# Kernel tuning notes

Hardware: AMD Instinct MI355X
Metric: run time of the kernel (lower is better)

The kernel has to match this reference:

```python
import jax, jax.numpy as jnp
import numpy as np

N_NODES = 100000
N_GRAPHS = 64
NEG_SLOPE = 0.1


def lrelu(x):
    return jnp.where(x > 0, x, NEG_SLOPE * x)


def gcn_layer(x, W, b, src, dst, deg_inv_sqrt):
    # PyG GCNConv: x' = D^-1/2 (A + I) D^-1/2 (x W) + b
    h = x @ W  # [N, out]
    norm = (deg_inv_sqrt[src] * deg_inv_sqrt[dst])[:, None]  # [E, 1]
    agg = jax.ops.segment_sum(h[src] * norm, dst, num_segments=N_NODES)
    agg = agg + h * (deg_inv_sqrt ** 2)[:, None]  # self-loop contribution
    return agg + b


def setup_inputs() -> dict:
    key = jax.random.key(0)
    ks = jax.random.split(key, 12)
    E = 1600000
    x = jax.random.normal(ks[0], (N_NODES, 128), dtype=jnp.float32)
    edge_index = jax.random.randint(ks[1], (2, E), 0, N_NODES, dtype=jnp.int32)
    batch = jnp.sort(jax.random.randint(ks[2], (N_NODES,), 0, N_GRAPHS, dtype=jnp.int32))

    def glorot(k, shape):
        fan_in, fan_out = shape
        s = jnp.sqrt(6.0 / (fan_in + fan_out))
        return jax.random.uniform(k, shape, jnp.float32, -s, s)

    return {
        "x": x,
        "edge_index": edge_index,
        "batch": batch,
        "W1": glorot(ks[3], (128, 32)),
        "b1": jnp.zeros((32,), jnp.float32),
        "W2": glorot(ks[4], (32, 64)),
        "b2": jnp.zeros((64,), jnp.float32),
        "Wl1": glorot(ks[5], (64, 128)),
        "bl1": jnp.zeros((128,), jnp.float32),
        "Wl2": glorot(ks[6], (128, 64)),
        "bl2": jnp.zeros((64,), jnp.float32),
        "Wl3": glorot(ks[7], (64, 1)),
        "bl3": jnp.zeros((1,), jnp.float32),
    }


def reference(x, edge_index, batch, W1, b1, W2, b2, Wl1, bl1, Wl2, bl2, Wl3, bl3):
    src, dst = edge_index[0], edge_index[1]
    # degree with self-loops (symmetric norm, all edge weights = 1)
    deg = jax.ops.segment_sum(jnp.ones_like(src, dtype=x.dtype), dst, num_segments=N_NODES) + 1.0
    deg_inv_sqrt = jax.lax.rsqrt(deg)

    h = lrelu(gcn_layer(x, W1, b1, src, dst, deg_inv_sqrt))
    h = gcn_layer(h, W2, b2, src, dst, deg_inv_sqrt)
    g = jax.ops.segment_max(h, batch, num_segments=N_GRAPHS)  # global max pool [G, 64]
    g = lrelu(g @ Wl1 + bl1)
    g = lrelu(g @ Wl2 + bl2)
    return g @ Wl3 + bl3  # [G, 1]
```

## Files before the change

kernel.cpp:

```cpp
#include <hip/hip_runtime.h>
#include <hip/hip_fp16.h>
#include <math.h>

#define N_NODES 100000
#define N_EDGES 1600000
#define N_GRAPHS 64
#define NB 391
#define CAP 5504

__device__ __forceinline__ unsigned f2o(float f) {
    unsigned u = __float_as_uint(f);
    return (u & 0x80000000u) ? ~u : (u | 0x80000000u);
}
__device__ __forceinline__ float o2f(unsigned u) {
    return (u & 0x80000000u) ? __uint_as_float(u & 0x7fffffffu) : __uint_as_float(~u);
}

__device__ __forceinline__ float4 cvt8(float2 raw) {
    __half2 h0 = ((const __half2*)&raw)[0];
    __half2 h1 = ((const __half2*)&raw)[1];
    float2 f0 = __half22float2(h0);
    float2 f1 = __half22float2(h1);
    return make_float4(f0.x, f0.y, f1.x, f1.y);
}
__device__ __forceinline__ float4 loadh8(const __half* p) {
    return cvt8(*(const float2*)p);
}
__device__ __forceinline__ void storeh8(__half* p, float4 v) {
    __half2 o0 = __floats2half2_rn(v.x, v.y);
    __half2 o1 = __floats2half2_rn(v.z, v.w);
    float2 ow;
    ((__half2*)&ow)[0] = o0;
    ((__half2*)&ow)[1] = o1;
    *(float2*)p = ow;
}

typedef _Float16 h2r __attribute__((ext_vector_type(2)));
typedef _Float16 h4  __attribute__((ext_vector_type(4)));
union HB { float4 f4; h2r h[4]; };
union H4 { float2 f2; h4 h; };

__global__ __launch_bounds__(256) void bucket_kernel(const int* __restrict__ src, const int* __restrict__ dst,
                                                     int* __restrict__ bucketCursor, unsigned* __restrict__ ebuf) {
    __shared__ int hist[NB];
    __shared__ int cur[NB];
    int tid = threadIdx.x;
    for (int b = tid; b < NB; b += 256) hist[b] = 0;
    __syncthreads();
    int e0 = blockIdx.x * 3200;
    for (int i = tid; i < 3200; i += 256) {
        int d = dst[e0 + i];
        atomicAdd(&hist[d >> 8], 1);
    }
    __syncthreads();
    for (int b = tid; b < NB; b += 256) {
        int h = hist[b];
        cur[b] = h ? atomicAdd(&bucketCursor[b], h) : 0;
    }
    __syncthreads();
    for (int i = tid; i < 3200; i += 256) {
        int d = dst[e0 + i];
        int s = src[e0 + i];
        int bu = d >> 8;
        int pos = atomicAdd(&cur[bu], 1);
        if (pos < CAP)
            ebuf[(size_t)bu * CAP + pos] = ((unsigned)(d & 255) << 24) | (unsigned)s;
    }
}

__global__ __launch_bounds__(256) void csr_kernel(const unsigned* __restrict__ ebuf,
                                                  const int* __restrict__ bucketCursor,
                                                  int* __restrict__ colb, int* __restrict__ rowptr,
                                                  int* __restrict__ cnt, float* __restrict__ dis) {
    __shared__ unsigned stage[CAP];
    __shared__ int c256[256], row256[256], cur256[256];
    int b = blockIdx.x;
    int tid = threadIdx.x;
    int M = bucketCursor[b];
    if (M > CAP) M = CAP;
    c256[tid] = 0;
    __syncthreads();
    const unsigned* eb = ebuf + (size_t)b * CAP;
    for (int i = tid; i < M; i += 256) atomicAdd(&c256[eb[i] >> 24], 1);
    __syncthreads();
    if (tid < 64) {
        int c0 = c256[tid * 4], c1 = c256[tid * 4 + 1], c2 = c256[tid * 4 + 2], c3 = c256[tid * 4 + 3];
        int s = c0 + c1 + c2 + c3;
        int inc = s;
        #pragma unroll
        for (int o = 1; o < 64; o <<= 1) {
            int v = __shfl_up(inc, o, 64);
            if (tid >= o) inc += v;
        }
        int ex = inc - s;
        row256[tid * 4] = ex;
        row256[tid * 4 + 1] = ex + c0;
        row256[tid * 4 + 2] = ex + c0 + c1;
        row256[tid * 4 + 3] = ex + c0 + c1 + c2;
    }
    __syncthreads();
    cur256[tid] = row256[tid];
    int node = (b << 8) + tid;
    if (node < N_NODES) {
        int c = c256[tid];
        cnt[node] = c;
        dis[node] = rsqrtf((float)(c + 1));
        rowptr[node] = b * CAP + row256[tid];
    }
    __syncthreads();
    for (int i = tid; i < M; i += 256) {
        unsigned p = eb[i];
        int slot = atomicAdd(&cur256[p >> 24], 1);
        stage[slot] = p & 0xFFFFFFu;
    }
    __syncthreads();
    for (int i = tid; i < M; i += 256) colb[b * CAP + i] = (int)stage[i];
}

__global__ __launch_bounds__(256) void gemm1_kernel(const float* __restrict__ x, const float* __restrict__ W1,
                                                    const float* __restrict__ dis, __half* __restrict__ hs1h) {
    __shared__ __half xsh[128][136];
    __shared__ __half wth[32][136];
    int tid = threadIdx.x;
    int r0 = blockIdx.x * 128;
    for (int idx = tid; idx < 128 * 32; idx += 256) {
        int k = idx >> 5, j = idx & 31;
        wth[j][k] = __float2half_rn(W1[idx]);
    }
    for (int idx = tid; idx < 128 * 32; idx += 256) {
        int r = idx >> 5, c4 = idx & 31;
        int gr = r0 + r;
        float4 v = (gr < N_NODES) ? ((const float4*)x)[(size_t)gr * 32 + c4] : make_float4(0.f, 0.f, 0.f, 0.f);
        __half* p = &xsh[r][c4 * 4];
        *(__half2*)p       = __floats2half2_rn(v.x, v.y);
        *(__half2*)(p + 2) = __floats2half2_rn(v.z, v.w);
    }
    __syncthreads();
    int jg = tid & 7;
    int rg = tid >> 3;
    float acc[4][4];
    #pragma unroll
    for (int i = 0; i < 4; i++)
        #pragma unroll
        for (int j = 0; j < 4; j++) acc[i][j] = 0.f;
    for (int kc = 0; kc < 128; kc += 8) {
        HB xr[4], wr[4];
        #pragma unroll
        for (int ri = 0; ri < 4; ri++) xr[ri].f4 = *(const float4*)&xsh[rg + 32 * ri][kc];
        #pragma unroll
        for (int jj = 0; jj < 4; jj++) wr[jj].f4 = *(const float4*)&wth[jg * 4 + jj][kc];
        #pragma unroll
        for (int ri = 0; ri < 4; ri++) {
            #pragma unroll
            for (int jj = 0; jj < 4; jj++) {
                #pragma unroll
                for (int t = 0; t < 4; t++) {
#if defined(__has_builtin) && __has_builtin(__builtin_amdgcn_fdot2)
                    acc[ri][jj] = __builtin_amdgcn_fdot2(xr[ri].h[t], wr[jj].h[t], acc[ri][jj], false);
#else
                    acc[ri][jj] += (float)xr[ri].h[t][0] * (float)wr[jj].h[t][0]
                                 + (float)xr[ri].h[t][1] * (float)wr[jj].h[t][1];
#endif
                }
            }
        }
    }
    #pragma unroll
    for (int ri = 0; ri < 4; ri++) {
        int gr = r0 + rg + 32 * ri;
        if (gr < N_NODES) {
            float dr = dis[gr];
            float2 ow;
            ((__half2*)&ow)[0] = __floats2half2_rn(dr * acc[ri][0], dr * acc[ri][1]);
            ((__half2*)&ow)[1] = __floats2half2_rn(dr * acc[ri][2], dr * acc[ri][3]);
            *(float2*)&hs1h[(size_t)gr * 32 + jg * 4] = ow;
        }
    }
}

__global__ __launch_bounds__(256) void agg1_kernel(const __half* __restrict__ hs1h, const int* __restrict__ colb,
                                                   const int* __restrict__ rowptr, const int* __restrict__ cnt,
                                                   const float* __restrict__ dis, const float* __restrict__ b1,
                                                   __half* __restrict__ t1h) {
    int tid = threadIdx.x;
    int wid = tid >> 6;
    int lane = tid & 63;
    int half = lane >> 5;
    int es = (lane >> 3) & 3;
    int q = lane & 7;
    int w = blockIdx.x * 4 + wid;
    int r0 = w * 4;

    H4 z; z.f2 = make_float2(0.f, 0.f);
    int r = r0 + half;
    int st = rowptr[r];
    int n = cnt[r];
    H4 pS = z, p0 = z, p1 = z, p2 = z, p3 = z, p4 = z, p5 = z;
    if (es == 0) pS.f2 = *(const float2*)(hs1h + (size_t)r * 32 + q * 4);
    {
        int e0 = es, e1 = 4 + es, e2 = 8 + es, e3 = 12 + es, e4 = 16 + es, e5 = 20 + es;
        if (e0 < n) p0.f2 = *(const float2*)(hs1h + (size_t)colb[st + e0] * 32 + q * 4);
        if (e1 < n) p1.f2 = *(const float2*)(hs1h + (size_t)colb[st + e1] * 32 + q * 4);
        if (e2 < n) p2.f2 = *(const float2*)(hs1h + (size_t)colb[st + e2] * 32 + q * 4);
        if (e3 < n) p3.f2 = *(const float2*)(hs1h + (size_t)colb[st + e3] * 32 + q * 4);
        if (e4 < n) p4.f2 = *(const float2*)(hs1h + (size_t)colb[st + e4] * 32 + q * 4);
        if (e5 < n) p5.f2 = *(const float2*)(hs1h + (size_t)colb[st + e5] * 32 + q * 4);
    }
    #pragma unroll
    for (int i = 0; i < 2; i++) {
        int rA = r;
        int stA = st, nA = n;
        H4 rS = pS, v0 = p0, v1 = p1, v2 = p2, v3 = p3, v4 = p4, v5 = p5;
        pS = z; p0 = z; p1 = z; p2 = z; p3 = z; p4 = z; p5 = z;
        if (i == 0) {
            r = r0 + 2 + half;
            st = rowptr[r];
            n = cnt[r];
            if (es == 0) pS.f2 = *(const float2*)(hs1h + (size_t)r * 32 + q * 4);
            int e0 = es, e1 = 4 + es, e2 = 8 + es, e3 = 12 + es, e4 = 16 + es, e5 = 20 + es;
            if (e0 < n) p0.f2 = *(const float2*)(hs1h + (size_t)colb[st + e0] * 32 + q * 4);
            if (e1 < n) p1.f2 = *(const float2*)(hs1h + (size_t)colb[st + e1] * 32 + q * 4);
            if (e2 < n) p2.f2 = *(const float2*)(hs1h + (size_t)colb[st + e2] * 32 + q * 4);
            if (e3 < n) p3.f2 = *(const float2*)(hs1h + (size_t)colb[st + e3] * 32 + q * 4);
            if (e4 < n) p4.f2 = *(const float2*)(hs1h + (size_t)colb[st + e4] * 32 + q * 4);
            if (e5 < n) p5.f2 = *(const float2*)(hs1h + (size_t)colb[st + e5] * 32 + q * 4);
        }
        h4 sh = (rS.h + (v0.h + v1.h)) + ((v2.h + v3.h) + (v4.h + v5.h));
        float4 a = make_float4((float)sh.x, (float)sh.y, (float)sh.z, (float)sh.w);
        for (int k = 24; k < nA; k += 8) {
            int e0 = k + es, e1 = k + 4 + es;
            if (e0 < nA) {
                float4 v = loadh8(hs1h + (size_t)colb[stA + e0] * 32 + q * 4);
                a.x += v.x; a.y += v.y; a.z += v.z; a.w += v.w;
            }
            if (e1 < nA) {
                float4 v = loadh8(hs1h + (size_t)colb[stA + e1] * 32 + q * 4);
                a.x += v.x; a.y += v.y; a.z += v.z; a.w += v.w;
            }
        }
        #pragma unroll
        for (int m = 8; m <= 16; m <<= 1) {
            a.x += __shfl_xor(a.x, m, 64);
            a.y += __shfl_xor(a.y, m, 64);
            a.z += __shfl_xor(a.z, m, 64);
            a.w += __shfl_xor(a.w, m, 64);
        }
        if (es == 0) {
            float4 bv = *(const float4*)&b1[q * 4];
            float dr = dis[rA];
            float4 v;
            v.x = dr * a.x + bv.x; v.y = dr * a.y + bv.y; v.z = dr * a.z + bv.z; v.w = dr * a.w + bv.w;
            v.x = v.x > 0.f ? v.x : 0.1f * v.x;
            v.y = v.y > 0.f ? v.y : 0.1f * v.y;
            v.z = v.z > 0.f ? v.z : 0.1f * v.z;
            v.w = v.w > 0.f ? v.w : 0.1f * v.w;
            v.x *= dr; v.y *= dr; v.z *= dr; v.w *= dr;
            storeh8(t1h + (size_t)rA * 32 + q * 4, v);
        }
    }
}

__global__ __launch_bounds__(1024) void agg2gemm_kernel(const __half* __restrict__ t1h, const int* __restrict__ colb,
                                                        const int* __restrict__ rowptr, const int* __restrict__ cnt,
                                                        const float* __restrict__ dis,
                                                        const float* __restrict__ W2, const float* __restrict__ b2,
                                                        const int* __restrict__ batch, unsigned* __restrict__ gbufu) {
    __shared__ float as1[64][32];
    __shared__ float w2s[32][64];
    __shared__ float red[16][64];
    int tid = threadIdx.x;
    int r0 = blockIdx.x * 64;
    for (int idx = tid; idx < 32 * 64; idx += 1024) w2s[idx >> 6][idx & 63] = W2[idx];

    int wid = tid >> 6;
    int lane = tid & 63;
    int half = lane >> 5;
    int es = (lane >> 3) & 3;
    int q = lane & 7;
    int base = r0 + wid * 4;

    H4 z; z.f2 = make_float2(0.f, 0.f);
    int r = base + half;
    bool vld = r < N_NODES;
    int st = vld ? rowptr[r] : 0;
    int n  = vld ? cnt[r] : 0;
    H4 pS = z, p0 = z, p1 = z, p2 = z, p3 = z, p4 = z, p5 = z;
    if (vld && es == 0) pS.f2 = *(const float2*)(t1h + (size_t)r * 32 + q * 4);
    {
        int e0 = es, e1 = 4 + es, e2 = 8 + es, e3 = 12 + es, e4 = 16 + es, e5 = 20 + es;
        if (e0 < n) p0.f2 = *(const float2*)(t1h + (size_t)colb[st + e0] * 32 + q * 4);
        if (e1 < n) p1.f2 = *(const float2*)(t1h + (size_t)colb[st + e1] * 32 + q * 4);
        if (e2 < n) p2.f2 = *(const float2*)(t1h + (size_t)colb[st + e2] * 32 + q * 4);
        if (e3 < n) p3.f2 = *(const float2*)(t1h + (size_t)colb[st + e3] * 32 + q * 4);
        if (e4 < n) p4.f2 = *(const float2*)(t1h + (size_t)colb[st + e4] * 32 + q * 4);
        if (e5 < n) p5.f2 = *(const float2*)(t1h + (size_t)colb[st + e5] * 32 + q * 4);
    }
    #pragma unroll
    for (int i = 0; i < 2; i++) {
        int rA = i * 2;
        int rAg = base + rA + half;
        bool vA = rAg < N_NODES;
        int stA = st, nA = n;
        H4 rS = pS, v0 = p0, v1 = p1, v2 = p2, v3 = p3, v4 = p4, v5 = p5;
        pS = z; p0 = z; p1 = z; p2 = z; p3 = z; p4 = z; p5 = z;
        if (i == 0) {
            r = base + 2 + half;
            vld = r < N_NODES;
            st = vld ? rowptr[r] : 0;
            n  = vld ? cnt[r] : 0;
            if (vld && es == 0) pS.f2 = *(const float2*)(t1h + (size_t)r * 32 + q * 4);
            int e0 = es, e1 = 4 + es, e2 = 8 + es, e3 = 12 + es, e4 = 16 + es, e5 = 20 + es;
            if (e0 < n) p0.f2 = *(const float2*)(t1h + (size_t)colb[st + e0] * 32 + q * 4);
            if (e1 < n) p1.f2 = *(const float2*)(t1h + (size_t)colb[st + e1] * 32 + q * 4);
            if (e2 < n) p2.f2 = *(const float2*)(t1h + (size_t)colb[st + e2] * 32 + q * 4);
            if (e3 < n) p3.f2 = *(const float2*)(t1h + (size_t)colb[st + e3] * 32 + q * 4);
            if (e4 < n) p4.f2 = *(const float2*)(t1h + (size_t)colb[st + e4] * 32 + q * 4);
            if (e5 < n) p5.f2 = *(const float2*)(t1h + (size_t)colb[st + e5] * 32 + q * 4);
        }
        h4 sh = (rS.h + (v0.h + v1.h)) + ((v2.h + v3.h) + (v4.h + v5.h));
        float4 a = make_float4((float)sh.x, (float)sh.y, (float)sh.z, (float)sh.w);
        for (int k = 24; k < nA; k += 8) {
            int e0 = k + es, e1 = k + 4 + es;
            if (e0 < nA) {
                float4 v = loadh8(t1h + (size_t)colb[stA + e0] * 32 + q * 4);
                a.x += v.x; a.y += v.y; a.z += v.z; a.w += v.w;
            }
            if (e1 < nA) {
                float4 v = loadh8(t1h + (size_t)colb[stA + e1] * 32 + q * 4);
                a.x += v.x; a.y += v.y; a.z += v.z; a.w += v.w;
            }
        }
        #pragma unroll
        for (int m = 8; m <= 16; m <<= 1) {
            a.x += __shfl_xor(a.x, m, 64);
            a.y += __shfl_xor(a.y, m, 64);
            a.z += __shfl_xor(a.z, m, 64);
            a.w += __shfl_xor(a.w, m, 64);
        }
        if (es == 0 && vA) {
            float dr = dis[rAg];
            float4 o = make_float4(dr * a.x, dr * a.y, dr * a.z, dr * a.w);
            *(float4*)&as1[wid * 4 + rA + half][q * 4] = o;
        }
    }
    __syncthreads();

    int j = tid & 63;
    int rq = tid >> 6;
    float w2c[32];
    #pragma unroll
    for (int k = 0; k < 32; k++) w2c[k] = w2s[k][j];
    float bj = b2[j];
    int rend = (r0 + 64 <= N_NODES) ? 64 : (N_NODES - r0);
    int gfirst = batch[r0];
    int glast = batch[r0 + rend - 1];
    bool uni = (gfirst == glast);
    float runmax = -INFINITY;
    #pragma unroll
    for (int i = 0; i < 4; i++) {
        int rl = rq + i * 16;
        if (rl >= rend) break;
        float acc = bj;
        #pragma unroll
        for (int kc = 0; kc < 32; kc += 4) {
            float4 av = *(const float4*)&as1[rl][kc];
            acc += av.x * w2c[kc] + av.y * w2c[kc + 1] + av.z * w2c[kc + 2] + av.w * w2c[kc + 3];
        }
        if (uni) runmax = fmaxf(runmax, acc);
        else atomicMax(&gbufu[batch[r0 + rl] * 64 + j], f2o(acc));
    }
    if (uni) {
        red[rq][j] = runmax;
        __syncthreads();
        if (tid < 64) {
            float m = -INFINITY;
            #pragma unroll
            for (int k = 0; k < 16; k++) m = fmaxf(m, red[k][tid]);
            atomicMax(&gbufu[gfirst * 64 + tid], f2o(m));
        }
    }
}

__global__ __launch_bounds__(256) void mlp_kernel(const unsigned* __restrict__ gbufu,
                                                  const float* __restrict__ Wl1, const float* __restrict__ bl1,
                                                  const float* __restrict__ Wl2, const float* __restrict__ bl2,
                                                  const float* __restrict__ Wl3, const float* __restrict__ bl3,
                                                  float* __restrict__ out) {
    __shared__ float A[64][64];
    __shared__ float B[64][128];
    int tid = threadIdx.x;
    for (int idx = tid; idx < 64 * 64; idx += 256) A[idx >> 6][idx & 63] = o2f(gbufu[idx]);
    __syncthreads();
    {
        int j = tid & 127;
        int rg = tid >> 7;
        float wc[64];
        #pragma unroll
        for (int k = 0; k < 64; k++) wc[k] = Wl1[k * 128 + j];
        float bj = bl1[j];
        for (int r = rg; r < 64; r += 2) {
            float acc = bj;
            #pragma unroll
            for (int kc = 0; kc < 64; kc += 4) {
                float4 av = *(const float4*)&A[r][kc];
                acc += av.x * wc[kc] + av.y * wc[kc + 1] + av.z * wc[kc + 2] + av.w * wc[kc + 3];
            }
            B[r][j] = acc > 0.f ? acc : 0.1f * acc;
        }
    }
    __syncthreads();
    {
        int j = tid & 63;
        int rg = tid >> 6;
        float wc[128];
        #pragma unroll
        for (int k = 0; k < 128; k++) wc[k] = Wl2[k * 64 + j];
        float bj = bl2[j];
        for (int r = rg; r < 64; r += 4) {
            float acc = bj;
            #pragma unroll
            for (int kc = 0; kc < 128; kc += 4) {
                float4 bv = *(const float4*)&B[r][kc];
                acc += bv.x * wc[kc] + bv.y * wc[kc + 1] + bv.z * wc[kc + 2] + bv.w * wc[kc + 3];
            }
            A[r][j] = acc > 0.f ? acc : 0.1f * acc;
        }
    }
    __syncthreads();
    if (tid < 64) {
        int r = tid;
        float acc = bl3[0];
        #pragma unroll
        for (int k = 0; k < 64; k++) acc += A[r][k] * Wl3[k];
        out[r] = acc;
    }
}

extern "C" void kernel_launch(void* const* d_in, const int* in_sizes, int n_in,
                              void* d_out, int out_size, void* d_ws, size_t ws_size,
                              hipStream_t stream) {
    (void)in_sizes; (void)n_in; (void)out_size; (void)ws_size;
    const float* x    = (const float*)d_in[0];
    const int*   edge = (const int*)d_in[1];
    const int*   batch= (const int*)d_in[2];
    const float* W1   = (const float*)d_in[3];
    const float* b1   = (const float*)d_in[4];
    const float* W2   = (const float*)d_in[5];
    const float* b2   = (const float*)d_in[6];
    const float* Wl1  = (const float*)d_in[7];
    const float* bl1  = (const float*)d_in[8];
    const float* Wl2  = (const float*)d_in[9];
    const float* bl2  = (const float*)d_in[10];
    const float* Wl3  = (const float*)d_in[11];
    const float* bl3  = (const float*)d_in[12];
    const int* srcp = edge;
    const int* dstp = edge + N_EDGES;

    char* ws = (char*)d_ws;
    int*      bucketCursor = (int*)ws;
    unsigned* gbufu        = (unsigned*)(bucketCursor + NB);
    size_t zeroed = (size_t)(NB + N_GRAPHS * 64) * 4;
    size_t off = (zeroed + 255) & ~(size_t)255;
    auto alloc = [&](size_t bytes) { char* p = ws + off; off = (off + bytes + 255) & ~(size_t)255; return p; };
    float*    dis    = (float*)alloc((size_t)N_NODES * 4);
    int*      cnt    = (int*)alloc((size_t)N_NODES * 4);
    int*      rowptr = (int*)alloc((size_t)N_NODES * 4);
    unsigned* ebuf   = (unsigned*)alloc((size_t)NB * CAP * 4);
    int*      colb   = (int*)alloc((size_t)NB * CAP * 4);
    __half*   hs1h   = (__half*)alloc((size_t)N_NODES * 32 * 2);
    __half*   t1h    = (__half*)alloc((size_t)N_NODES * 32 * 2);

    hipMemsetAsync(ws, 0, zeroed, stream);

    bucket_kernel  <<<500, 256, 0, stream>>>(srcp, dstp, bucketCursor, ebuf);
    csr_kernel     <<<NB, 256, 0, stream>>>(ebuf, bucketCursor, colb, rowptr, cnt, dis);
    gemm1_kernel   <<<(N_NODES + 127) / 128, 256, 0, stream>>>(x, W1, dis, hs1h);
    agg1_kernel    <<<6250, 256, 0, stream>>>(hs1h, colb, rowptr, cnt, dis, b1, t1h);
    agg2gemm_kernel<<<(N_NODES + 63) / 64, 1024, 0, stream>>>(t1h, colb, rowptr, cnt, dis, W2, b2, batch, gbufu);
    mlp_kernel     <<<1, 256, 0, stream>>>(gbufu, Wl1, bl1, Wl2, bl2, Wl3, bl3, (float*)d_out);
}
```

Measured before the change: 261.5 us.

## Split 32-wide half feature arrays into two 16-wide halves for gathers

Stores the layer-1 hidden features and the layer-1 output as two separate 16-column half-precision arrays instead of one 32-column array. The aggregation kernels now gather each half in a separate pass, using 4 lanes per row and 8 edges in parallel. The intent is a smaller per-pass gather working set (1.6 MB per half) that fits better in cache and raises edge-level parallelism. In exchange, colb indices are read twice and each gather is a narrower 32-byte access, so the number of random row fetches doubles.

```diff
diff --git a/kernel.cpp b/kernel.cpp
--- a/kernel.cpp
+++ b/kernel.cpp
@@ -118,7 +118,8 @@
 }
 
 __global__ __launch_bounds__(256) void gemm1_kernel(const float* __restrict__ x, const float* __restrict__ W1,
-                                                    const float* __restrict__ dis, __half* __restrict__ hs1h) {
+                                                    const float* __restrict__ dis,
+                                                    __half* __restrict__ ha, __half* __restrict__ hb) {
     __shared__ __half xsh[128][136];
     __shared__ __half wth[32][136];
     int tid = threadIdx.x;
@@ -165,6 +166,8 @@
             }
         }
     }
+    __half* hp = (jg < 4) ? ha : hb;
+    int q4 = (jg & 3) * 4;
     #pragma unroll
     for (int ri = 0; ri < 4; ri++) {
         int gr = r0 + rg + 32 * ri;
@@ -173,81 +176,77 @@
             float2 ow;
             ((__half2*)&ow)[0] = __floats2half2_rn(dr * acc[ri][0], dr * acc[ri][1]);
             ((__half2*)&ow)[1] = __floats2half2_rn(dr * acc[ri][2], dr * acc[ri][3]);
-            *(float2*)&hs1h[(size_t)gr * 32 + jg * 4] = ow;
-        }
-    }
-}
-
-__global__ __launch_bounds__(256) void agg1_kernel(const __half* __restrict__ hs1h, const int* __restrict__ colb,
+            *(float2*)&hp[(size_t)gr * 16 + q4] = ow;
+        }
+    }
+}
+
+__global__ __launch_bounds__(256) void agg1_kernel(const __half* __restrict__ ha, const __half* __restrict__ hb,
+                                                   const int* __restrict__ colb,
                                                    const int* __restrict__ rowptr, const int* __restrict__ cnt,
                                                    const float* __restrict__ dis, const float* __restrict__ b1,
-                                                   __half* __restrict__ t1h) {
+                                                   __half* __restrict__ ta, __half* __restrict__ tb) {
     int tid = threadIdx.x;
     int wid = tid >> 6;
     int lane = tid & 63;
     int half = lane >> 5;
-    int es = (lane >> 3) & 3;
-    int q = lane & 7;
+    int es = (lane >> 2) & 7;
+    int q = lane & 3;
     int w = blockIdx.x * 4 + wid;
     int r0 = w * 4;
 
+    int rI[2]  = { r0 + half, r0 + 2 + half };
+    int stI[2] = { rowptr[rI[0]], rowptr[rI[1]] };
+    int nI[2]  = { cnt[rI[0]], cnt[rI[1]] };
+    float dI[2] = { dis[rI[0]], dis[rI[1]] };
+
     H4 z; z.f2 = make_float2(0.f, 0.f);
-    int r = r0 + half;
-    int st = rowptr[r];
-    int n = cnt[r];
-    H4 pS = z, p0 = z, p1 = z, p2 = z, p3 = z, p4 = z, p5 = z;
-    if (es == 0) pS.f2 = *(const float2*)(hs1h + (size_t)r * 32 + q * 4);
+    H4 pS = z, p0 = z, p1 = z, p2 = z;
     {
-        int e0 = es, e1 = 4 + es, e2 = 8 + es, e3 = 12 + es, e4 = 16 + es, e5 = 20 + es;
-        if (e0 < n) p0.f2 = *(const float2*)(hs1h + (size_t)colb[st + e0] * 32 + q * 4);
-        if (e1 < n) p1.f2 = *(const float2*)(hs1h + (size_t)colb[st + e1] * 32 + q * 4);
-        if (e2 < n) p2.f2 = *(const float2*)(hs1h + (size_t)colb[st + e2] * 32 + q * 4);
-        if (e3 < n) p3.f2 = *(const float2*)(hs1h + (size_t)colb[st + e3] * 32 + q * 4);
-        if (e4 < n) p4.f2 = *(const float2*)(hs1h + (size_t)colb[st + e4] * 32 + q * 4);
-        if (e5 < n) p5.f2 = *(const float2*)(hs1h + (size_t)colb[st + e5] * 32 + q * 4);
-    }
-    #pragma unroll
-    for (int i = 0; i < 2; i++) {
-        int rA = r;
-        int stA = st, nA = n;
-        H4 rS = pS, v0 = p0, v1 = p1, v2 = p2, v3 = p3, v4 = p4, v5 = p5;
-        pS = z; p0 = z; p1 = z; p2 = z; p3 = z; p4 = z; p5 = z;
-        if (i == 0) {
-            r = r0 + 2 + half;
-            st = rowptr[r];
-            n = cnt[r];
-            if (es == 0) pS.f2 = *(const float2*)(hs1h + (size_t)r * 32 + q * 4);
-            int e0 = es, e1 = 4 + es, e2 = 8 + es, e3 = 12 + es, e4 = 16 + es, e5 = 20 + es;
-            if (e0 < n) p0.f2 = *(const float2*)(hs1h + (size_t)colb[st + e0] * 32 + q * 4);
-            if (e1 < n) p1.f2 = *(const float2*)(hs1h + (size_t)colb[st + e1] * 32 + q * 4);
-            if (e2 < n) p2.f2 = *(const float2*)(hs1h + (size_t)colb[st + e2] * 32 + q * 4);
-            if (e3 < n) p3.f2 = *(const float2*)(hs1h + (size_t)colb[st + e3] * 32 + q * 4);
-            if (e4 < n) p4.f2 = *(const float2*)(hs1h + (size_t)colb[st + e4] * 32 + q * 4);
-            if (e5 < n) p5.f2 = *(const float2*)(hs1h + (size_t)colb[st + e5] * 32 + q * 4);
-        }
-        h4 sh = (rS.h + (v0.h + v1.h)) + ((v2.h + v3.h) + (v4.h + v5.h));
+        int st = stI[0], n = nI[0];
+        if (es == 0) pS.f2 = *(const float2*)(ha + (size_t)rI[0] * 16 + q * 4);
+        int e0 = es, e1 = 8 + es, e2 = 16 + es;
+        if (e0 < n) p0.f2 = *(const float2*)(ha + (size_t)colb[st + e0] * 16 + q * 4);
+        if (e1 < n) p1.f2 = *(const float2*)(ha + (size_t)colb[st + e1] * 16 + q * 4);
+        if (e2 < n) p2.f2 = *(const float2*)(ha + (size_t)colb[st + e2] * 16 + q * 4);
+    }
+    #pragma unroll
+    for (int s = 0; s < 4; ++s) {
+        int it = s & 1;
+        const __half* gpA = (s >> 1) ? hb : ha;
+        int stA = stI[it], nA = nI[it], rA = rI[it];
+        float drA = dI[it];
+        H4 rS = pS, v0 = p0, v1 = p1, v2 = p2;
+        pS = z; p0 = z; p1 = z; p2 = z;
+        if (s < 3) {
+            int itn = (s + 1) & 1;
+            const __half* gp = ((s + 1) >> 1) ? hb : ha;
+            int st = stI[itn], n = nI[itn];
+            if (es == 0) pS.f2 = *(const float2*)(gp + (size_t)rI[itn] * 16 + q * 4);
+            int e0 = es, e1 = 8 + es, e2 = 16 + es;
+            if (e0 < n) p0.f2 = *(const float2*)(gp + (size_t)colb[st + e0] * 16 + q * 4);
+            if (e1 < n) p1.f2 = *(const float2*)(gp + (size_t)colb[st + e1] * 16 + q * 4);
+            if (e2 < n) p2.f2 = *(const float2*)(gp + (size_t)colb[st + e2] * 16 + q * 4);
+        }
+        h4 sh = (rS.h + (v0.h + v1.h)) + v2.h;
         float4 a = make_float4((float)sh.x, (float)sh.y, (float)sh.z, (float)sh.w);
         for (int k = 24; k < nA; k += 8) {
-            int e0 = k + es, e1 = k + 4 + es;
-            if (e0 < nA) {
-                float4 v = loadh8(hs1h + (size_t)colb[stA + e0] * 32 + q * 4);
+            int e = k + es;
+            if (e < nA) {
+                float4 v = loadh8(gpA + (size_t)colb[stA + e] * 16 + q * 4);
                 a.x += v.x; a.y += v.y; a.z += v.z; a.w += v.w;
             }
-            if (e1 < nA) {
-                float4 v = loadh8(hs1h + (size_t)colb[stA + e1] * 32 + q * 4);
-                a.x += v.x; a.y += v.y; a.z += v.z; a.w += v.w;
-            }
-        }
-        #pragma unroll
-        for (int m = 8; m <= 16; m <<= 1) {
+        }
+        #pragma unroll
+        for (int m = 4; m <= 16; m <<= 1) {
             a.x += __shfl_xor(a.x, m, 64);
             a.y += __shfl_xor(a.y, m, 64);
             a.z += __shfl_xor(a.z, m, 64);
             a.w += __shfl_xor(a.w, m, 64);
         }
         if (es == 0) {
-            float4 bv = *(const float4*)&b1[q * 4];
-            float dr = dis[rA];
+            float4 bv = *(const float4*)&b1[((s >> 1) << 4) + q * 4];
+            float dr = drA;
             float4 v;
             v.x = dr * a.x + bv.x; v.y = dr * a.y + bv.y; v.z = dr * a.z + bv.z; v.w = dr * a.w + bv.w;
             v.x = v.x > 0.f ? v.x : 0.1f * v.x;
@@ -255,12 +254,14 @@
             v.z = v.z > 0.f ? v.z : 0.1f * v.z;
             v.w = v.w > 0.f ? v.w : 0.1f * v.w;
             v.x *= dr; v.y *= dr; v.z *= dr; v.w *= dr;
-            storeh8(t1h + (size_t)rA * 32 + q * 4, v);
-        }
-    }
-}
-
-__global__ __launch_bounds__(1024) void agg2gemm_kernel(const __half* __restrict__ t1h, const int* __restrict__ colb,
+            __half* op = ((s >> 1) ? tb : ta) + (size_t)rA * 16 + q * 4;
+            storeh8(op, v);
+        }
+    }
+}
+
+__global__ __launch_bounds__(1024) void agg2gemm_kernel(const __half* __restrict__ ta, const __half* __restrict__ tb,
+                                                        const int* __restrict__ colb,
                                                         const int* __restrict__ rowptr, const int* __restrict__ cnt,
                                                         const float* __restrict__ dis,
                                                         const float* __restrict__ W2, const float* __restrict__ b2,
@@ -275,72 +276,65 @@
     int wid = tid >> 6;
     int lane = tid & 63;
     int half = lane >> 5;
-    int es = (lane >> 3) & 3;
-    int q = lane & 7;
+    int es = (lane >> 2) & 7;
+    int q = lane & 3;
     int base = r0 + wid * 4;
 
+    int rI[2]  = { base + half, base + 2 + half };
+    bool vI[2] = { rI[0] < N_NODES, rI[1] < N_NODES };
+    int stI[2] = { vI[0] ? rowptr[rI[0]] : 0, vI[1] ? rowptr[rI[1]] : 0 };
+    int nI[2]  = { vI[0] ? cnt[rI[0]] : 0,   vI[1] ? cnt[rI[1]] : 0 };
+    float dI[2] = { vI[0] ? dis[rI[0]] : 0.f, vI[1] ? dis[rI[1]] : 0.f };
+
     H4 z; z.f2 = make_float2(0.f, 0.f);
-    int r = base + half;
-    bool vld = r < N_NODES;
-    int st = vld ? rowptr[r] : 0;
-    int n  = vld ? cnt[r] : 0;
-    H4 pS = z, p0 = z, p1 = z, p2 = z, p3 = z, p4 = z, p5 = z;
-    if (vld && es == 0) pS.f2 = *(const float2*)(t1h + (size_t)r * 32 + q * 4);
+    H4 pS = z, p0 = z, p1 = z, p2 = z;
     {
-        int e0 = es, e1 = 4 + es, e2 = 8 + es, e3 = 12 + es, e4 = 16 + es, e5 = 20 + es;
-        if (e0 < n) p0.f2 = *(const float2*)(t1h + (size_t)colb[st + e0] * 32 + q * 4);
-        if (e1 < n) p1.f2 = *(const float2*)(t1h + (size_t)colb[st + e1] * 32 + q * 4);
-        if (e2 < n) p2.f2 = *(const float2*)(t1h + (size_t)colb[st + e2] * 32 + q * 4);
-        if (e3 < n) p3.f2 = *(const float2*)(t1h + (size_t)colb[st + e3] * 32 + q * 4);
-        if (e4 < n) p4.f2 = *(const float2*)(t1h + (size_t)colb[st + e4] * 32 + q * 4);
-        if (e5 < n) p5.f2 = *(const float2*)(t1h + (size_t)colb[st + e5] * 32 + q * 4);
-    }
-    #pragma unroll
-    for (int i = 0; i < 2; i++) {
-        int rA = i * 2;
-        int rAg = base + rA + half;
-        bool vA = rAg < N_NODES;
-        int stA = st, nA = n;
-        H4 rS = pS, v0 = p0, v1 = p1, v2 = p2, v3 = p3, v4 = p4, v5 = p5;
-        pS = z; p0 = z; p1 = z; p2 = z; p3 = z; p4 = z; p5 = z;
-        if (i == 0) {
-            r = base + 2 + half;
-            vld = r < N_NODES;
-            st = vld ? rowptr[r] : 0;
-            n  = vld ? cnt[r] : 0;
-            if (vld && es == 0) pS.f2 = *(const float2*)(t1h + (size_t)r * 32 + q * 4);
-            int e0 = es, e1 = 4 + es, e2 = 8 + es, e3 = 12 + es, e4 = 16 + es, e5 = 20 + es;
-            if (e0 < n) p0.f2 = *(const float2*)(t1h + (size_t)colb[st + e0] * 32 + q * 4);
-            if (e1 < n) p1.f2 = *(const float2*)(t1h + (size_t)colb[st + e1] * 32 + q * 4);
-            if (e2 < n) p2.f2 = *(const float2*)(t1h + (size_t)colb[st + e2] * 32 + q * 4);
-            if (e3 < n) p3.f2 = *(const float2*)(t1h + (size_t)colb[st + e3] * 32 + q * 4);
-            if (e4 < n) p4.f2 = *(const float2*)(t1h + (size_t)colb[st + e4] * 32 + q * 4);
-            if (e5 < n) p5.f2 = *(const float2*)(t1h + (size_t)colb[st + e5] * 32 + q * 4);
-        }
-        h4 sh = (rS.h + (v0.h + v1.h)) + ((v2.h + v3.h) + (v4.h + v5.h));
+        int st = stI[0], n = nI[0];
+        if (vI[0] && es == 0) pS.f2 = *(const float2*)(ta + (size_t)rI[0] * 16 + q * 4);
+        int e0 = es, e1 = 8 + es, e2 = 16 + es;
+        if (e0 < n) p0.f2 = *(const float2*)(ta + (size_t)colb[st + e0] * 16 + q * 4);
+        if (e1 < n) p1.f2 = *(const float2*)(ta + (size_t)colb[st + e1] * 16 + q * 4);
+        if (e2 < n) p2.f2 = *(const float2*)(ta + (size_t)colb[st + e2] * 16 + q * 4);
+    }
+    #pragma unroll
+    for (int s = 0; s < 4; ++s) {
+        int it = s & 1;
+        const __half* gpA = (s >> 1) ? tb : ta;
+        int stA = stI[it], nA = nI[it], rA = rI[it];
+        bool vA = vI[it];
+        float drA = dI[it];
+        H4 rS = pS, v0 = p0, v1 = p1, v2 = p2;
+        pS = z; p0 = z; p1 = z; p2 = z;
+        if (s < 3) {
+            int itn = (s + 1) & 1;
+            const __half* gp = ((s + 1) >> 1) ? tb : ta;
+            int st = stI[itn], n = nI[itn];
+            if (vI[itn] && es == 0) pS.f2 = *(const float2*)(gp + (size_t)rI[itn] * 16 + q * 4);
+            int e0 = es, e1 = 8 + es, e2 = 16 + es;
+            if (e0 < n) p0.f2 = *(const float2*)(gp + (size_t)colb[st + e0] * 16 + q * 4);
+            if (e1 < n) p1.f2 = *(const float2*)(gp + (size_t)colb[st + e1] * 16 + q * 4);
+            if (e2 < n) p2.f2 = *(const float2*)(gp + (size_t)colb[st + e2] * 16 + q * 4);
+        }
+        h4 sh = (rS.h + (v0.h + v1.h)) + v2.h;
         float4 a = make_float4((float)sh.x, (float)sh.y, (float)sh.z, (float)sh.w);
         for (int k = 24; k < nA; k += 8) {
-            int e0 = k + es, e1 = k + 4 + es;
-            if (e0 < nA) {
-                float4 v = loadh8(t1h + (size_t)colb[stA + e0] * 32 + q * 4);
+            int e = k + es;
+            if (e < nA) {
+                float4 v = loadh8(gpA + (size_t)colb[stA + e] * 16 + q * 4);
                 a.x += v.x; a.y += v.y; a.z += v.z; a.w += v.w;
             }
-            if (e1 < nA) {
-                float4 v = loadh8(t1h + (size_t)colb[stA + e1] * 32 + q * 4);
-                a.x += v.x; a.y += v.y; a.z += v.z; a.w += v.w;
-            }
-        }
-        #pragma unroll
-        for (int m = 8; m <= 16; m <<= 1) {
+        }
+        #pragma unroll
+        for (int m = 4; m <= 16; m <<= 1) {
             a.x += __shfl_xor(a.x, m, 64);
             a.y += __shfl_xor(a.y, m, 64);
             a.z += __shfl_xor(a.z, m, 64);
             a.w += __shfl_xor(a.w, m, 64);
         }
         if (es == 0 && vA) {
-            float dr = dis[rAg];
+            float dr = drA;
             float4 o = make_float4(dr * a.x, dr * a.y, dr * a.z, dr * a.w);
-            *(float4*)&as1[wid * 4 + rA + half][q * 4] = o;
+            *(float4*)&as1[rA - r0][((s >> 1) << 4) + q * 4] = o;
         }
     }
     __syncthreads();
@@ -467,15 +461,17 @@
     int*      rowptr = (int*)alloc((size_t)N_NODES * 4);
     unsigned* ebuf   = (unsigned*)alloc((size_t)NB * CAP * 4);
     int*      colb   = (int*)alloc((size_t)NB * CAP * 4);
-    __half*   hs1h   = (__half*)alloc((size_t)N_NODES * 32 * 2);
-    __half*   t1h    = (__half*)alloc((size_t)N_NODES * 32 * 2);
+    __half*   ha     = (__half*)alloc((size_t)N_NODES * 16 * 2);
+    __half*   hb     = (__half*)alloc((size_t)N_NODES * 16 * 2);
+    __half*   ta     = (__half*)alloc((size_t)N_NODES * 16 * 2);
+    __half*   tb     = (__half*)alloc((size_t)N_NODES * 16 * 2);
 
     hipMemsetAsync(ws, 0, zeroed, stream);
 
     bucket_kernel  <<<500, 256, 0, stream>>>(srcp, dstp, bucketCursor, ebuf);
     csr_kernel     <<<NB, 256, 0, stream>>>(ebuf, bucketCursor, colb, rowptr, cnt, dis);
-    gemm1_kernel   <<<(N_NODES + 127) / 128, 256, 0, stream>>>(x, W1, dis, hs1h);
-    agg1_kernel    <<<6250, 256, 0, stream>>>(hs1h, colb, rowptr, cnt, dis, b1, t1h);
-    agg2gemm_kernel<<<(N_NODES + 63) / 64, 1024, 0, stream>>>(t1h, colb, rowptr, cnt, dis, W2, b2, batch, gbufu);
+    gemm1_kernel   <<<(N_NODES + 127) / 128, 256, 0, stream>>>(x, W1, dis, ha, hb);
+    agg1_kernel    <<<6250, 256, 0, stream>>>(ha, hb, colb, rowptr, cnt, dis, b1, ta, tb);
+    agg2gemm_kernel<<<(N_NODES + 63) / 64, 1024, 0, stream>>>(ta, tb, colb, rowptr, cnt, dis, W2, b2, batch, gbufu);
     mlp_kernel     <<<1, 256, 0, stream>>>(gbufu, Wl1, bl1, Wl2, bl2, Wl3, bl3, (float*)d_out);
 }
```

After: 276.7 us. +5.8%, slower.

## Merge prep kernels via cooperative grid sync and fold MLP into last block

Applied to the files above, without the earlier changes.

Replaces the bucket, CSR and gemm1 kernels with one cooperative kernel that separates the phases with grid-wide syncs, sharing LDS through a union. The final MLP kernel is folded into agg2gemm: a global done-counter lets the last block read the pooled maxima and run the MLP. This removes several kernel launches and their inter-kernel gaps. In exchange it adds grid-sync overhead, limits the gemm phase to 500 blocks looping over tiles, and serializes the MLP tail on one block.

```diff
diff --git a/kernel.cpp b/kernel.cpp
--- a/kernel.cpp
+++ b/kernel.cpp
@@ -1,6 +1,9 @@
 #include <hip/hip_runtime.h>
 #include <hip/hip_fp16.h>
+#include <hip/hip_cooperative_groups.h>
 #include <math.h>
+
+namespace cg = cooperative_groups;
 
 #define N_NODES 100000
 #define N_EDGES 1600000
@@ -40,140 +43,148 @@
 union HB { float4 f4; h2r h[4]; };
 union H4 { float2 f2; h4 h; };
 
-__global__ __launch_bounds__(256) void bucket_kernel(const int* __restrict__ src, const int* __restrict__ dst,
-                                                     int* __restrict__ bucketCursor, unsigned* __restrict__ ebuf) {
-    __shared__ int hist[NB];
-    __shared__ int cur[NB];
+struct PrepLDS {
+    union {
+        struct { int hist[NB]; int cur[NB]; } a;
+        struct { unsigned stage[CAP]; int c256[256]; int row256[256]; int cur256[256]; } b;
+        struct { __half xsh[128][136]; __half wth[32][136]; } c;
+    };
+};
+
+__global__ __launch_bounds__(256) void prep_kernel(const int* __restrict__ src, const int* __restrict__ dst,
+                                                   const float* __restrict__ x, const float* __restrict__ W1,
+                                                   int* __restrict__ bucketCursor, unsigned* __restrict__ ebuf,
+                                                   int* __restrict__ colb, int* __restrict__ rowptr,
+                                                   int* __restrict__ cnt, float* __restrict__ dis,
+                                                   __half* __restrict__ hs1h) {
+    __shared__ PrepLDS L;
+    cg::grid_group grid = cg::this_grid();
     int tid = threadIdx.x;
-    for (int b = tid; b < NB; b += 256) hist[b] = 0;
-    __syncthreads();
-    int e0 = blockIdx.x * 3200;
-    for (int i = tid; i < 3200; i += 256) {
-        int d = dst[e0 + i];
-        atomicAdd(&hist[d >> 8], 1);
-    }
-    __syncthreads();
-    for (int b = tid; b < NB; b += 256) {
-        int h = hist[b];
-        cur[b] = h ? atomicAdd(&bucketCursor[b], h) : 0;
-    }
-    __syncthreads();
-    for (int i = tid; i < 3200; i += 256) {
-        int d = dst[e0 + i];
-        int s = src[e0 + i];
-        int bu = d >> 8;
-        int pos = atomicAdd(&cur[bu], 1);
-        if (pos < CAP)
-            ebuf[(size_t)bu * CAP + pos] = ((unsigned)(d & 255) << 24) | (unsigned)s;
-    }
-}
-
-__global__ __launch_bounds__(256) void csr_kernel(const unsigned* __restrict__ ebuf,
-                                                  const int* __restrict__ bucketCursor,
-                                                  int* __restrict__ colb, int* __restrict__ rowptr,
-                                                  int* __restrict__ cnt, float* __restrict__ dis) {
-    __shared__ unsigned stage[CAP];
-    __shared__ int c256[256], row256[256], cur256[256];
-    int b = blockIdx.x;
-    int tid = threadIdx.x;
-    int M = bucketCursor[b];
-    if (M > CAP) M = CAP;
-    c256[tid] = 0;
-    __syncthreads();
-    const unsigned* eb = ebuf + (size_t)b * CAP;
-    for (int i = tid; i < M; i += 256) atomicAdd(&c256[eb[i] >> 24], 1);
-    __syncthreads();
-    if (tid < 64) {
-        int c0 = c256[tid * 4], c1 = c256[tid * 4 + 1], c2 = c256[tid * 4 + 2], c3 = c256[tid * 4 + 3];
-        int s = c0 + c1 + c2 + c3;
-        int inc = s;
+
+    {
+        for (int b = tid; b < NB; b += 256) L.a.hist[b] = 0;
+        __syncthreads();
+        int e0 = blockIdx.x * 3200;
+        for (int i = tid; i < 3200; i += 256) {
+            int d = dst[e0 + i];
+            atomicAdd(&L.a.hist[d >> 8], 1);
+        }
+        __syncthreads();
+        for (int b = tid; b < NB; b += 256) {
+            int h = L.a.hist[b];
+            L.a.cur[b] = h ? atomicAdd(&bucketCursor[b], h) : 0;
+        }
+        __syncthreads();
+        for (int i = tid; i < 3200; i += 256) {
+            int d = dst[e0 + i];
+            int s = src[e0 + i];
+            int bu = d >> 8;
+            int pos = atomicAdd(&L.a.cur[bu], 1);
+            if (pos < CAP)
+                ebuf[(size_t)bu * CAP + pos] = ((unsigned)(d & 255) << 24) | (unsigned)s;
+        }
+    }
+    grid.sync();
+
+    if (blockIdx.x < NB) {
+        int b = blockIdx.x;
+        int M = bucketCursor[b];
+        if (M > CAP) M = CAP;
+        L.b.c256[tid] = 0;
+        __syncthreads();
+        const unsigned* eb = ebuf + (size_t)b * CAP;
+        for (int i = tid; i < M; i += 256) atomicAdd(&L.b.c256[eb[i] >> 24], 1);
+        __syncthreads();
+        if (tid < 64) {
+            int c0 = L.b.c256[tid * 4], c1 = L.b.c256[tid * 4 + 1], c2 = L.b.c256[tid * 4 + 2], c3 = L.b.c256[tid * 4 + 3];
+            int s = c0 + c1 + c2 + c3;
+            int inc = s;
+            #pragma unroll
+            for (int o = 1; o < 64; o <<= 1) {
+                int v = __shfl_up(inc, o, 64);
+                if (tid >= o) inc += v;
+            }
+            int ex = inc - s;
+            L.b.row256[tid * 4] = ex;
+            L.b.row256[tid * 4 + 1] = ex + c0;
+            L.b.row256[tid * 4 + 2] = ex + c0 + c1;
+            L.b.row256[tid * 4 + 3] = ex + c0 + c1 + c2;
+        }
+        __syncthreads();
+        L.b.cur256[tid] = L.b.row256[tid];
+        int node = (b << 8) + tid;
+        if (node < N_NODES) {
+            int c = L.b.c256[tid];
+            cnt[node] = c;
+            dis[node] = rsqrtf((float)(c + 1));
+            rowptr[node] = b * CAP + L.b.row256[tid];
+        }
+        __syncthreads();
+        for (int i = tid; i < M; i += 256) {
+            unsigned p = eb[i];
+            int slot = atomicAdd(&L.b.cur256[p >> 24], 1);
+            L.b.stage[slot] = p & 0xFFFFFFu;
+        }
+        __syncthreads();
+        for (int i = tid; i < M; i += 256) colb[b * CAP + i] = (int)L.b.stage[i];
+    }
+    grid.sync();
+
+    for (int t = blockIdx.x; t < (N_NODES + 127) / 128; t += 500) {
+        __syncthreads();
+        int r0 = t * 128;
+        for (int idx = tid; idx < 128 * 32; idx += 256) {
+            int k = idx >> 5, j = idx & 31;
+            L.c.wth[j][k] = __float2half_rn(W1[idx]);
+        }
+        for (int idx = tid; idx < 128 * 32; idx += 256) {
+            int r = idx >> 5, c4 = idx & 31;
+            int gr = r0 + r;
+            float4 v = (gr < N_NODES) ? ((const float4*)x)[(size_t)gr * 32 + c4] : make_float4(0.f, 0.f, 0.f, 0.f);
+            __half* p = &L.c.xsh[r][c4 * 4];
+            *(__half2*)p       = __floats2half2_rn(v.x, v.y);
+            *(__half2*)(p + 2) = __floats2half2_rn(v.z, v.w);
+        }
+        __syncthreads();
+        int jg = tid & 7;
+        int rg = tid >> 3;
+        float acc[4][4];
         #pragma unroll
-        for (int o = 1; o < 64; o <<= 1) {
-            int v = __shfl_up(inc, o, 64);
-            if (tid >= o) inc += v;
-        }
-        int ex = inc - s;
-        row256[tid * 4] = ex;
-        row256[tid * 4 + 1] = ex + c0;
-        row256[tid * 4 + 2] = ex + c0 + c1;
-        row256[tid * 4 + 3] = ex + c0 + c1 + c2;
-    }
-    __syncthreads();
-    cur256[tid] = row256[tid];
-    int node = (b << 8) + tid;
-    if (node < N_NODES) {
-        int c = c256[tid];
-        cnt[node] = c;
-        dis[node] = rsqrtf((float)(c + 1));
-        rowptr[node] = b * CAP + row256[tid];
-    }
-    __syncthreads();
-    for (int i = tid; i < M; i += 256) {
-        unsigned p = eb[i];
-        int slot = atomicAdd(&cur256[p >> 24], 1);
-        stage[slot] = p & 0xFFFFFFu;
-    }
-    __syncthreads();
-    for (int i = tid; i < M; i += 256) colb[b * CAP + i] = (int)stage[i];
-}
-
-__global__ __launch_bounds__(256) void gemm1_kernel(const float* __restrict__ x, const float* __restrict__ W1,
-                                                    const float* __restrict__ dis, __half* __restrict__ hs1h) {
-    __shared__ __half xsh[128][136];
-    __shared__ __half wth[32][136];
-    int tid = threadIdx.x;
-    int r0 = blockIdx.x * 128;
-    for (int idx = tid; idx < 128 * 32; idx += 256) {
-        int k = idx >> 5, j = idx & 31;
-        wth[j][k] = __float2half_rn(W1[idx]);
-    }
-    for (int idx = tid; idx < 128 * 32; idx += 256) {
-        int r = idx >> 5, c4 = idx & 31;
-        int gr = r0 + r;
-        float4 v = (gr < N_NODES) ? ((const float4*)x)[(size_t)gr * 32 + c4] : make_float4(0.f, 0.f, 0.f, 0.f);
-        __half* p = &xsh[r][c4 * 4];
-        *(__half2*)p       = __floats2half2_rn(v.x, v.y);
-        *(__half2*)(p + 2) = __floats2half2_rn(v.z, v.w);
-    }
-    __syncthreads();
-    int jg = tid & 7;
-    int rg = tid >> 3;
-    float acc[4][4];
-    #pragma unroll
-    for (int i = 0; i < 4; i++)
-        #pragma unroll
-        for (int j = 0; j < 4; j++) acc[i][j] = 0.f;
-    for (int kc = 0; kc < 128; kc += 8) {
-        HB xr[4], wr[4];
-        #pragma unroll
-        for (int ri = 0; ri < 4; ri++) xr[ri].f4 = *(const float4*)&xsh[rg + 32 * ri][kc];
-        #pragma unroll
-        for (int jj = 0; jj < 4; jj++) wr[jj].f4 = *(const float4*)&wth[jg * 4 + jj][kc];
+        for (int i = 0; i < 4; i++)
+            #pragma unroll
+            for (int j = 0; j < 4; j++) acc[i][j] = 0.f;
+        for (int kc = 0; kc < 128; kc += 8) {
+            HB xr[4], wr[4];
+            #pragma unroll
+            for (int ri = 0; ri < 4; ri++) xr[ri].f4 = *(const float4*)&L.c.xsh[rg + 32 * ri][kc];
+            #pragma unroll
+            for (int jj = 0; jj < 4; jj++) wr[jj].f4 = *(const float4*)&L.c.wth[jg * 4 + jj][kc];
+            #pragma unroll
+            for (int ri = 0; ri < 4; ri++) {
+                #pragma unroll
+                for (int jj = 0; jj < 4; jj++) {
+                    #pragma unroll
+                    for (int tt = 0; tt < 4; tt++) {
+#if defined(__has_builtin) && __has_builtin(__builtin_amdgcn_fdot2)
+                        acc[ri][jj] = __builtin_amdgcn_fdot2(xr[ri].h[tt], wr[jj].h[tt], acc[ri][jj], false);
+#else
+                        acc[ri][jj] += (float)xr[ri].h[tt][0] * (float)wr[jj].h[tt][0]
+                                     + (float)xr[ri].h[tt][1] * (float)wr[jj].h[tt][1];
+#endif
+                    }
+                }
+            }
+        }
         #pragma unroll
         for (int ri = 0; ri < 4; ri++) {
-            #pragma unroll
-            for (int jj = 0; jj < 4; jj++) {
-                #pragma unroll
-                for (int t = 0; t < 4; t++) {
-#if defined(__has_builtin) && __has_builtin(__builtin_amdgcn_fdot2)
-                    acc[ri][jj] = __builtin_amdgcn_fdot2(xr[ri].h[t], wr[jj].h[t], acc[ri][jj], false);
-#else
-                    acc[ri][jj] += (float)xr[ri].h[t][0] * (float)wr[jj].h[t][0]
-                                 + (float)xr[ri].h[t][1] * (float)wr[jj].h[t][1];
-#endif
-                }
-            }
-        }
-    }
-    #pragma unroll
-    for (int ri = 0; ri < 4; ri++) {
-        int gr = r0 + rg + 32 * ri;
-        if (gr < N_NODES) {
-            float dr = dis[gr];
-            float2 ow;
-            ((__half2*)&ow)[0] = __floats2half2_rn(dr * acc[ri][0], dr * acc[ri][1]);
-            ((__half2*)&ow)[1] = __floats2half2_rn(dr * acc[ri][2], dr * acc[ri][3]);
-            *(float2*)&hs1h[(size_t)gr * 32 + jg * 4] = ow;
+            int gr = r0 + rg + 32 * ri;
+            if (gr < N_NODES) {
+                float dr = dis[gr];
+                float2 ow;
+                ((__half2*)&ow)[0] = __floats2half2_rn(dr * acc[ri][0], dr * acc[ri][1]);
+                ((__half2*)&ow)[1] = __floats2half2_rn(dr * acc[ri][2], dr * acc[ri][3]);
+                *(float2*)&hs1h[(size_t)gr * 32 + jg * 4] = ow;
+            }
         }
     }
 }
@@ -260,17 +271,28 @@
     }
 }
 
+struct A2L {
+    union {
+        struct { float as1[64][32]; float w2s[32][64]; float red[16][64]; } g;
+        struct { float A[64][64]; float B[64][128]; } m;
+    };
+};
+
 __global__ __launch_bounds__(1024) void agg2gemm_kernel(const __half* __restrict__ t1h, const int* __restrict__ colb,
                                                         const int* __restrict__ rowptr, const int* __restrict__ cnt,
                                                         const float* __restrict__ dis,
                                                         const float* __restrict__ W2, const float* __restrict__ b2,
-                                                        const int* __restrict__ batch, unsigned* __restrict__ gbufu) {
-    __shared__ float as1[64][32];
-    __shared__ float w2s[32][64];
-    __shared__ float red[16][64];
+                                                        const int* __restrict__ batch, unsigned* __restrict__ gbufu,
+                                                        unsigned* __restrict__ donecnt,
+                                                        const float* __restrict__ Wl1, const float* __restrict__ bl1,
+                                                        const float* __restrict__ Wl2, const float* __restrict__ bl2,
+                                                        const float* __restrict__ Wl3, const float* __restrict__ bl3,
+                                                        float* __restrict__ out) {
+    __shared__ A2L L;
+    __shared__ int finL;
     int tid = threadIdx.x;
     int r0 = blockIdx.x * 64;
-    for (int idx = tid; idx < 32 * 64; idx += 1024) w2s[idx >> 6][idx & 63] = W2[idx];
+    for (int idx = tid; idx < 32 * 64; idx += 1024) L.g.w2s[idx >> 6][idx & 63] = W2[idx];
 
     int wid = tid >> 6;
     int lane = tid & 63;
@@ -340,7 +362,7 @@
         if (es == 0 && vA) {
             float dr = dis[rAg];
             float4 o = make_float4(dr * a.x, dr * a.y, dr * a.z, dr * a.w);
-            *(float4*)&as1[wid * 4 + rA + half][q * 4] = o;
+            *(float4*)&L.g.as1[wid * 4 + rA + half][q * 4] = o;
         }
     }
     __syncthreads();
@@ -349,7 +371,7 @@
     int rq = tid >> 6;
     float w2c[32];
     #pragma unroll
-    for (int k = 0; k < 32; k++) w2c[k] = w2s[k][j];
+    for (int k = 0; k < 32; k++) w2c[k] = L.g.w2s[k][j];
     float bj = b2[j];
     int rend = (r0 + 64 <= N_NODES) ? 64 : (N_NODES - r0);
     int gfirst = batch[r0];
@@ -363,76 +385,89 @@
         float acc = bj;
         #pragma unroll
         for (int kc = 0; kc < 32; kc += 4) {
-            float4 av = *(const float4*)&as1[rl][kc];
+            float4 av = *(const float4*)&L.g.as1[rl][kc];
             acc += av.x * w2c[kc] + av.y * w2c[kc + 1] + av.z * w2c[kc + 2] + av.w * w2c[kc + 3];
         }
         if (uni) runmax = fmaxf(runmax, acc);
         else atomicMax(&gbufu[batch[r0 + rl] * 64 + j], f2o(acc));
     }
     if (uni) {
-        red[rq][j] = runmax;
+        L.g.red[rq][j] = runmax;
         __syncthreads();
         if (tid < 64) {
             float m = -INFINITY;
             #pragma unroll
-            for (int k = 0; k < 16; k++) m = fmaxf(m, red[k][tid]);
+            for (int k = 0; k < 16; k++) m = fmaxf(m, L.g.red[k][tid]);
             atomicMax(&gbufu[gfirst * 64 + tid], f2o(m));
         }
     }
-}
-
-__global__ __launch_bounds__(256) void mlp_kernel(const unsigned* __restrict__ gbufu,
-                                                  const float* __restrict__ Wl1, const float* __restrict__ bl1,
-                                                  const float* __restrict__ Wl2, const float* __restrict__ bl2,
-                                                  const float* __restrict__ Wl3, const float* __restrict__ bl3,
-                                                  float* __restrict__ out) {
-    __shared__ float A[64][64];
-    __shared__ float B[64][128];
-    int tid = threadIdx.x;
-    for (int idx = tid; idx < 64 * 64; idx += 256) A[idx >> 6][idx & 63] = o2f(gbufu[idx]);
+
     __syncthreads();
-    {
-        int j = tid & 127;
-        int rg = tid >> 7;
-        float wc[64];
-        #pragma unroll
-        for (int k = 0; k < 64; k++) wc[k] = Wl1[k * 128 + j];
-        float bj = bl1[j];
-        for (int r = rg; r < 64; r += 2) {
-            float acc = bj;
-            #pragma unroll
-            for (int kc = 0; kc < 64; kc += 4) {
-                float4 av = *(const float4*)&A[r][kc];
-                acc += av.x * wc[kc] + av.y * wc[kc + 1] + av.z * wc[kc + 2] + av.w * wc[kc + 3];
-            }
-            B[r][j] = acc > 0.f ? acc : 0.1f * acc;
-        }
+    if (tid == 0) {
+        __threadfence();
+        unsigned p = atomicAdd(donecnt, 1u);
+        finL = (p == gridDim.x - 1) ? 1 : 0;
     }
     __syncthreads();
-    {
-        int j = tid & 63;
-        int rg = tid >> 6;
-        float wc[128];
-        #pragma unroll
-        for (int k = 0; k < 128; k++) wc[k] = Wl2[k * 64 + j];
-        float bj = bl2[j];
-        for (int r = rg; r < 64; r += 4) {
-            float acc = bj;
-            #pragma unroll
-            for (int kc = 0; kc < 128; kc += 4) {
-                float4 bv = *(const float4*)&B[r][kc];
-                acc += bv.x * wc[kc] + bv.y * wc[kc + 1] + bv.z * wc[kc + 2] + bv.w * wc[kc + 3];
-            }
-            A[r][j] = acc > 0.f ? acc : 0.1f * acc;
-        }
-    }
-    __syncthreads();
-    if (tid < 64) {
-        int r = tid;
-        float acc = bl3[0];
-        #pragma unroll
-        for (int k = 0; k < 64; k++) acc += A[r][k] * Wl3[k];
-        out[r] = acc;
+    if (finL) {
+        for (int idx = tid; idx < 64 * 64; idx += 1024) {
+            unsigned u = atomicMax(&gbufu[idx], 0u);
+            L.m.A[idx >> 6][idx & 63] = o2f(u);
+        }
+        __syncthreads();
+        {
+            int jj = tid & 127, rg = tid >> 7;
+            float acc[8];
+            #pragma unroll
+            for (int i = 0; i < 8; i++) acc[i] = bl1[jj];
+            for (int c = 0; c < 4; c++) {
+                float wc[16];
+                #pragma unroll
+                for (int k = 0; k < 16; k++) wc[k] = Wl1[(c * 16 + k) * 128 + jj];
+                #pragma unroll
+                for (int i = 0; i < 8; i++) {
+                    int rr = rg + 8 * i;
+                    #pragma unroll
+                    for (int k = 0; k < 16; k++) acc[i] += L.m.A[rr][c * 16 + k] * wc[k];
+                }
+            }
+            #pragma unroll
+            for (int i = 0; i < 8; i++) {
+                float v = acc[i];
+                L.m.B[rg + 8 * i][jj] = v > 0.f ? v : 0.1f * v;
+            }
+        }
+        __syncthreads();
+        {
+            int jj = tid & 63, rg = tid >> 6;
+            float acc[4];
+            #pragma unroll
+            for (int i = 0; i < 4; i++) acc[i] = bl2[jj];
+            for (int c = 0; c < 8; c++) {
+                float wc[16];
+                #pragma unroll
+                for (int k = 0; k < 16; k++) wc[k] = Wl2[(c * 16 + k) * 64 + jj];
+                #pragma unroll
+                for (int i = 0; i < 4; i++) {
+                    int rr = rg + 16 * i;
+                    #pragma unroll
+                    for (int k = 0; k < 16; k++) acc[i] += L.m.B[rr][c * 16 + k] * wc[k];
+                }
+            }
+            __syncthreads();
+            #pragma unroll
+            for (int i = 0; i < 4; i++) {
+                float v = acc[i];
+                L.m.A[rg + 16 * i][jj] = v > 0.f ? v : 0.1f * v;
+            }
+        }
+        __syncthreads();
+        if (tid < 64) {
+            float acc = bl3[0];
+            #pragma unroll
+            for (int k = 0; k < 64; k++) acc += L.m.A[tid][k] * Wl3[k];
+            out[tid] = acc;
+        }
     }
 }
 
@@ -459,7 +494,8 @@
     char* ws = (char*)d_ws;
     int*      bucketCursor = (int*)ws;
     unsigned* gbufu        = (unsigned*)(bucketCursor + NB);
-    size_t zeroed = (size_t)(NB + N_GRAPHS * 64) * 4;
+    unsigned* donecnt      = gbufu + N_GRAPHS * 64;
+    size_t zeroed = (size_t)(NB + N_GRAPHS * 64 + 1) * 4;
     size_t off = (zeroed + 255) & ~(size_t)255;
     auto alloc = [&](size_t bytes) { char* p = ws + off; off = (off + bytes + 255) & ~(size_t)255; return p; };
     float*    dis    = (float*)alloc((size_t)N_NODES * 4);
@@ -472,10 +508,14 @@
 
     hipMemsetAsync(ws, 0, zeroed, stream);
 
-    bucket_kernel  <<<500, 256, 0, stream>>>(srcp, dstp, bucketCursor, ebuf);
-    csr_kernel     <<<NB, 256, 0, stream>>>(ebuf, bucketCursor, colb, rowptr, cnt, dis);
-    gemm1_kernel   <<<(N_NODES + 127) / 128, 256, 0, stream>>>(x, W1, dis, hs1h);
-    agg1_kernel    <<<6250, 256, 0, stream>>>(hs1h, colb, rowptr, cnt, dis, b1, t1h);
-    agg2gemm_kernel<<<(N_NODES + 63) / 64, 1024, 0, stream>>>(t1h, colb, rowptr, cnt, dis, W2, b2, batch, gbufu);
-    mlp_kernel     <<<1, 256, 0, stream>>>(gbufu, Wl1, bl1, Wl2, bl2, Wl3, bl3, (float*)d_out);
-}
+    void* pargs[] = { (void*)&srcp, (void*)&dstp, (void*)&x, (void*)&W1,
+                      (void*)&bucketCursor, (void*)&ebuf, (void*)&colb,
+                      (void*)&rowptr, (void*)&cnt, (void*)&dis, (void*)&hs1h };
+    hipLaunchCooperativeKernel((void*)prep_kernel, dim3(500), dim3(256), pargs, 0, stream);
+
+    agg1_kernel<<<6250, 256, 0, stream>>>(hs1h, colb, rowptr, cnt, dis, b1, t1h);
+
+    agg2gemm_kernel<<<(N_NODES + 63) / 64, 1024, 0, stream>>>(t1h, colb, rowptr, cnt, dis, W2, b2, batch,
+                                                              gbufu, donecnt, Wl1, bl1, Wl2, bl2, Wl3, bl3,
+                                                              (float*)d_out);
+}
```

Result: slower. 443.1 us (+69.5%).
